# Performance work log

Hardware: AMD Instinct MI355X
Metric: run time of the kernel (lower is better)

Reference implementation:

```python
import jax, jax.numpy as jnp
import numpy as np

NBITS = 8
NUM_HEADS = 6


def _quant(x, alpha, nbits=NBITS):
    # LSQ-style fake quantization with straight-through estimator.
    qn = -(2 ** (nbits - 1))        # -128
    qp = 2 ** (nbits - 1) - 1       # 127
    s = jnp.clip(x / alpha, qn, qp)
    s = s + jax.lax.stop_gradient(jnp.round(s) - s)  # STE round
    return s * alpha


def setup_inputs() -> dict:
    key = jax.random.key(0)
    ks = jax.random.split(key, 12)
    B, N, C = 2, 2048, 384
    x = jax.random.normal(ks[0], (B, N, C), dtype=jnp.float32)
    w_qkv = jax.random.normal(ks[1], (3 * C, C), dtype=jnp.float32) * 0.02
    w_proj = jax.random.normal(ks[2], (C, C), dtype=jnp.float32) * 0.02
    b_proj = jnp.zeros((C,), dtype=jnp.float32)

    def alpha(k, lo, hi):
        return jax.random.uniform(k, (1,), dtype=jnp.float32, minval=lo, maxval=hi)

    return {
        "x": x,
        "w_qkv": w_qkv,
        "w_proj": w_proj,
        "b_proj": b_proj,
        "a_qkv_w": alpha(ks[3], 0.001, 0.005),
        "a_qkv_a": alpha(ks[4], 0.02, 0.05),
        "a_proj_w": alpha(ks[5], 0.001, 0.005),
        "a_proj_a": alpha(ks[6], 0.02, 0.05),
        "a_q": alpha(ks[7], 0.01, 0.03),
        "a_k": alpha(ks[8], 0.01, 0.03),
        "a_v": alpha(ks[9], 0.01, 0.03),
        "a_attn": alpha(ks[10], 0.01, 0.03),
        "a_attn2": alpha(ks[11], 0.005, 0.01),
    }


def reference(x, w_qkv, w_proj, b_proj, a_qkv_w, a_qkv_a, a_proj_w, a_proj_a,
              a_q, a_k, a_v, a_attn, a_attn2):
    B, N, C = x.shape
    H = NUM_HEADS
    D = C // H
    scale = D ** (-0.5)

    # quantized qkv linear (no bias)
    qkv = _quant(x, a_qkv_a) @ _quant(w_qkv, a_qkv_w).T          # [B,N,3C]
    qkv = qkv.reshape(B, N, 3, H, D).transpose(2, 0, 3, 1, 4)    # [3,B,H,N,D]
    q, k, v = qkv[0], qkv[1], qkv[2]
    q = _quant(q, a_q)
    k = _quant(k, a_k)
    v = _quant(v, a_v)

    attn = jnp.einsum("bhnd,bhmd->bhnm", q, k) * scale           # [B,H,N,N]
    attn = _quant(attn, a_attn)
    attn = jax.nn.softmax(attn, axis=-1)
    attn = _quant(attn, a_attn2)

    out = jnp.einsum("bhnm,bhmd->bhnd", attn, v)                 # [B,H,N,D]
    out = out.transpose(0, 2, 1, 3).reshape(B, N, C)

    # quantized output projection (with bias)
    out = _quant(out, a_proj_a) @ _quant(w_proj, a_proj_w).T + b_proj
    return out
```

## Files before the change

kernel.cpp:

```cpp
#include <hip/hip_runtime.h>
#include <math.h>


typedef int i32x4 __attribute__((ext_vector_type(4)));

#define MFMA_I8(a, b, c) __builtin_amdgcn_mfma_i32_16x16x64_i8(a, b, c, 0, 0, 0)

__device__ __forceinline__ float qclip(float s) {
  return fminf(fmaxf(s, -128.0f), 127.0f);
}

__device__ __forceinline__ float fdivn(float x, float c, float rc) {
  float q0 = x * rc;
  float e = fmaf(-c, q0, x);
  return fmaf(e, rc, q0);
}

__device__ __forceinline__ void quant16_body(const float* __restrict__ in,
                                             signed char* __restrict__ out,
                                             float a, int i) {
  const float4* p = (const float4*)in + 4 * (size_t)i;
  union { uint4 u; signed char c[16]; } o;
#pragma unroll
  for (int u = 0; u < 4; ++u) {
    float4 v = p[u];
    o.c[4 * u + 0] = (signed char)(int)rintf(qclip(v.x / a));
    o.c[4 * u + 1] = (signed char)(int)rintf(qclip(v.y / a));
    o.c[4 * u + 2] = (signed char)(int)rintf(qclip(v.z / a));
    o.c[4 * u + 3] = (signed char)(int)rintf(qclip(v.w / a));
  }
  *(uint4*)(out + 16 * (size_t)i) = o.u;
}

__global__ __launch_bounds__(256)
void prep(const float* __restrict__ x, const float* __restrict__ wqkv,
          const float* __restrict__ wproj,
          signed char* __restrict__ xq, signed char* __restrict__ wqq,
          signed char* __restrict__ wpq, float* __restrict__ E2,
          const float* __restrict__ a_qkv_a, const float* __restrict__ a_qkv_w,
          const float* __restrict__ a_proj_w, const float* __restrict__ aattn) {
  const int b = blockIdx.x, t = threadIdx.x;
  if (b < 384) {
    int i = b * 256 + t;
    if (i < 98304) quant16_body(x, xq, a_qkv_a[0], i);
  } else if (b < 492) {
    int i = (b - 384) * 256 + t;
    if (i < 27648) quant16_body(wqkv, wqq, a_qkv_w[0], i);
  } else if (b < 528) {
    int i = (b - 492) * 256 + t;
    if (i < 9216) quant16_body(wproj, wpq, a_proj_w[0], i);
  } else {
    int i = (b - 528) * 256 + t;
    float a = aattn[0];
    int vm = (i >> 8) - 128;
    int s = (i & 255) - 128;
    float m = a * (float)vm;
    E2[i] = expf(a * (float)s - m);
  }
}

__global__ __launch_bounds__(256)
void gemm_qkv(const signed char* __restrict__ A, const signed char* __restrict__ W,
              signed char* __restrict__ qws, signed char* __restrict__ kws,
              signed char* __restrict__ vwsT,
              const float* __restrict__ aa, const float* __restrict__ aw,
              const float* __restrict__ aq, const float* __restrict__ ak,
              const float* __restrict__ av) {
  const int t = threadIdx.x;
  const int w = t >> 6, lane = t & 63;
  const int lm = lane & 15, quad = lane >> 4;
  const int wm = w >> 1, wn = w & 1;
  const int m0 = blockIdx.x * 128 + wm * 64;
  const int n0 = blockIdx.y * 128 + wn * 64;
  i32x4 acc[4][4] = {};
  for (int k0 = 0; k0 < 384; k0 += 64) {
    i32x4 af[4], bf[4];
#pragma unroll
    for (int mt = 0; mt < 4; ++mt)
      af[mt] = *(const i32x4*)(A + (size_t)(m0 + mt * 16 + lm) * 384 + k0 + quad * 16);
#pragma unroll
    for (int nt = 0; nt < 4; ++nt)
      bf[nt] = *(const i32x4*)(W + (size_t)(n0 + nt * 16 + lm) * 384 + k0 + quad * 16);
#pragma unroll
    for (int mt = 0; mt < 4; ++mt)
#pragma unroll
      for (int nt = 0; nt < 4; ++nt)
        acc[mt][nt] = MFMA_I8(af[mt], bf[nt], acc[mt][nt]);
  }
  const float sAB = aa[0] * aw[0];
  const float vaq = aq[0], vak = ak[0], vav = av[0];
#pragma unroll
  for (int mt = 0; mt < 4; ++mt) {
#pragma unroll
    for (int nt = 0; nt < 4; ++nt) {
      int cg = n0 + nt * 16 + lm;
      int t3 = cg / 384;
      int rem = cg - t3 * 384;
      int h = rem >> 6, d = rem & 63;
#pragma unroll
      for (int r = 0; r < 4; ++r) {
        int m = m0 + mt * 16 + quad * 4 + r;
        int bb = m >> 11, nn = m & 2047;
        int bh = bb * 6 + h;
        float val = (float)acc[mt][nt][r] * sAB;
        if (t3 == 0) {
          qws[((size_t)(bh * 2048 + nn) << 6) + d] = (signed char)(int)rintf(qclip(val / vaq));
        } else if (t3 == 1) {
          kws[((size_t)(bh * 2048 + nn) << 6) + d] = (signed char)(int)rintf(qclip(val / vak));
        } else {
          vwsT[((size_t)((bh << 6) + d) << 11) + nn] = (signed char)(int)rintf(qclip(val / vav));
        }
      }
    }
  }
}

#define TROW 2064
__global__ __launch_bounds__(256)
void attn_fused(const signed char* __restrict__ qws, const signed char* __restrict__ kws,
                const signed char* __restrict__ vwsT, const float* __restrict__ E2,
                signed char* __restrict__ ows,
                const float* __restrict__ aq, const float* __restrict__ ak,
                const float* __restrict__ aattn, const float* __restrict__ aattn2,
                const float* __restrict__ av, const float* __restrict__ apa) {
  __shared__ signed char tileS[16 * TROW];
  __shared__ float EfS[16 * 257];
  const int t = threadIdx.x;
  const int w = t >> 6, lane = t & 63;
  const int lm = lane & 15, quad = lane >> 4;
  const int i0 = blockIdx.x * 16;
  const int bh = blockIdx.y;

  const signed char* Qb = qws + ((size_t)bh << 17);
  const signed char* Kb = kws + ((size_t)bh << 17);

  i32x4 bq = *(const i32x4*)(Qb + ((size_t)(i0 + lm) << 6) + quad * 16);
  const float sc = aq[0] * ak[0] * 0.125f;
  const float ia = aattn[0];
  const float ria = 1.0f / ia;
#pragma unroll 4
  for (int ct = 0; ct < 32; ++ct) {
    int col0 = (w << 9) + ct * 16;
    i32x4 akf = *(const i32x4*)(Kb + ((size_t)(col0 + lm) << 6) + quad * 16);
    i32x4 z = {};
    i32x4 acc = MFMA_I8(akf, bq, z);
    union { unsigned int u; signed char c[4]; } pk;
#pragma unroll
    for (int r = 0; r < 4; ++r) {
      float sv = (float)acc[r] * sc;
      pk.c[r] = (signed char)(int)rintf(qclip(fdivn(sv, ia, ria)));
    }
    *(unsigned int*)(tileS + lm * TROW + col0 + quad * 4) = pk.u;
  }
  __syncthreads();

  const float a2 = aattn2[0];
  int* lutI = (int*)EfS;
#pragma unroll
  for (int rr = 0; rr < 4; ++rr) {
    const int row = w * 4 + rr;
    const char4* prow = (const char4*)(tileS + row * TROW);
    char4 vals[8];
    int vmax = -129;
#pragma unroll
    for (int u = 0; u < 8; ++u) {
      vals[u] = prow[lane + (u << 6)];
      vmax = max(vmax, (int)vals[u].x);
      vmax = max(vmax, (int)vals[u].y);
      vmax = max(vmax, (int)vals[u].z);
      vmax = max(vmax, (int)vals[u].w);
    }
#pragma unroll
    for (int off = 32; off > 0; off >>= 1)
      vmax = max(vmax, __shfl_xor(vmax, off, 64));
    float efu[4];
#pragma unroll
    for (int u = 0; u < 4; ++u) {
      efu[u] = E2[((vmax + 128) << 8) + u * 64 + lane];
      EfS[row * 257 + u * 64 + lane] = efu[u];
    }
    const float* Er = EfS + row * 257 + 128;
    float l = 0.0f;
#pragma unroll
    for (int u = 0; u < 8; ++u) {
      l += Er[(int)vals[u].x];
      l += Er[(int)vals[u].y];
      l += Er[(int)vals[u].z];
      l += Er[(int)vals[u].w];
    }
#pragma unroll
    for (int off = 32; off > 0; off >>= 1)
      l += __shfl_xor(l, off, 64);
#pragma unroll
    for (int u = 0; u < 4; ++u) {
      int pq = (int)(signed char)(int)rintf(qclip(efu[u] / l / a2));
      lutI[row * 257 + u * 64 + lane] = pq;
    }
  }
  __syncthreads();

  i32x4 areg[8];
  {
    const int* lr = lutI + lm * 257 + 128;
    const signed char* srow = tileS + lm * TROW + (w << 9) + quad * 16;
#pragma unroll
    for (int js = 0; js < 8; ++js) {
      union { uint4 u; signed char c[16]; } sv;
      sv.u = *(const uint4*)(srow + js * 64);
      union { i32x4 v; signed char c[16]; } dv;
#pragma unroll
      for (int b = 0; b < 16; ++b) dv.c[b] = (signed char)lr[(int)sv.c[b]];
      areg[js] = dv.v;
    }
  }

  const signed char* Vb = vwsT + ((size_t)bh << 17) + (w << 9);
  i32x4 acc[4] = {};
#pragma unroll
  for (int js = 0; js < 8; ++js) {
    int j0 = js * 64;
    i32x4 bf[4];
#pragma unroll
    for (int nt = 0; nt < 4; ++nt)
      bf[nt] = *(const i32x4*)(Vb + ((size_t)(nt * 16 + lm) << 11) + j0 + quad * 16);
#pragma unroll
    for (int nt = 0; nt < 4; ++nt)
      acc[nt] = MFMA_I8(areg[js], bf[nt], acc[nt]);
  }

  int* red = (int*)tileS;
  __syncthreads();
  if (w > 0) {
    int* rw = red + (w - 1) * 1088 + lane * 17;
#pragma unroll
    for (int nt = 0; nt < 4; ++nt)
#pragma unroll
      for (int r = 0; r < 4; ++r)
        rw[nt * 4 + r] = acc[nt][r];
  }
  __syncthreads();
  if (w == 0) {
    const float so = a2 * av[0];
    const float ipa = apa[0];
    int bb = bh / 6, h = bh % 6;
#pragma unroll
    for (int nt = 0; nt < 4; ++nt) {
      int d = nt * 16 + lm;
#pragma unroll
      for (int r = 0; r < 4; ++r) {
        int s = acc[nt][r] + red[lane * 17 + nt * 4 + r]
              + red[1088 + lane * 17 + nt * 4 + r]
              + red[2176 + lane * 17 + nt * 4 + r];
        int i = i0 + quad * 4 + r;
        ows[(size_t)((bb << 11) + i) * 384 + (h << 6) + d] =
            (signed char)(int)rintf(qclip((float)s * so / ipa));
      }
    }
  }
}

__global__ __launch_bounds__(256)
void gemm_proj(const signed char* __restrict__ A, const signed char* __restrict__ W,
               const float* __restrict__ bias, float* __restrict__ out,
               const float* __restrict__ apa, const float* __restrict__ apw) {
  const int t = threadIdx.x;
  const int w = t >> 6, lane = t & 63;
  const int lm = lane & 15, quad = lane >> 4;
  const int wm = w >> 1, wn = w & 1;
  const int m0 = blockIdx.x * 64 + wm * 32;
  const int n0 = blockIdx.y * 64 + wn * 32;
  i32x4 acc[2][2] = {};
  for (int k0 = 0; k0 < 384; k0 += 64) {
    i32x4 af[2], bf[2];
#pragma unroll
    for (int mt = 0; mt < 2; ++mt)
      af[mt] = *(const i32x4*)(A + (size_t)(m0 + mt * 16 + lm) * 384 + k0 + quad * 16);
#pragma unroll
    for (int nt = 0; nt < 2; ++nt)
      bf[nt] = *(const i32x4*)(W + (size_t)(n0 + nt * 16 + lm) * 384 + k0 + quad * 16);
#pragma unroll
    for (int mt = 0; mt < 2; ++mt)
#pragma unroll
      for (int nt = 0; nt < 2; ++nt)
        acc[mt][nt] = MFMA_I8(af[mt], bf[nt], acc[mt][nt]);
  }
  const float sAB = apa[0] * apw[0];
#pragma unroll
  for (int mt = 0; mt < 2; ++mt) {
#pragma unroll
    for (int nt = 0; nt < 2; ++nt) {
      int cg = n0 + nt * 16 + lm;
#pragma unroll
      for (int r = 0; r < 4; ++r) {
        int m = m0 + mt * 16 + quad * 4 + r;
        out[(size_t)m * 384 + cg] = (float)acc[mt][nt][r] * sAB + bias[cg];
      }
    }
  }
}

extern "C" void kernel_launch(void* const* d_in, const int* in_sizes, int n_in,
                              void* d_out, int out_size, void* d_ws, size_t ws_size,
                              hipStream_t stream) {
  const float* x        = (const float*)d_in[0];
  const float* w_qkv    = (const float*)d_in[1];
  const float* w_proj   = (const float*)d_in[2];
  const float* b_proj   = (const float*)d_in[3];
  const float* a_qkv_w  = (const float*)d_in[4];
  const float* a_qkv_a  = (const float*)d_in[5];
  const float* a_proj_w = (const float*)d_in[6];
  const float* a_proj_a = (const float*)d_in[7];
  const float* a_q      = (const float*)d_in[8];
  const float* a_k      = (const float*)d_in[9];
  const float* a_v      = (const float*)d_in[10];
  const float* a_attn   = (const float*)d_in[11];
  const float* a_attn2  = (const float*)d_in[12];

  char* wsb = (char*)d_ws;
  signed char* xq   = (signed char*)(wsb + 0);
  signed char* wqq  = (signed char*)(wsb + 1572864);
  signed char* wpq  = (signed char*)(wsb + 2015232);
  signed char* qws  = (signed char*)(wsb + 2162688);
  signed char* kws  = (signed char*)(wsb + 3735552);
  signed char* vwsT = (signed char*)(wsb + 5308416);
  signed char* ows  = (signed char*)(wsb + 6881280);
  float*       E2   = (float*)(wsb + 8454144);

  prep<<<784, 256, 0, stream>>>(x, w_qkv, w_proj, xq, wqq, wpq, E2,
                                a_qkv_a, a_qkv_w, a_proj_w, a_attn);
  gemm_qkv<<<dim3(32, 9), 256, 0, stream>>>(xq, wqq, qws, kws, vwsT,
                                            a_qkv_a, a_qkv_w, a_q, a_k, a_v);
  attn_fused<<<dim3(128, 12), 256, 0, stream>>>(qws, kws, vwsT, E2, ows,
                                                a_q, a_k, a_attn, a_attn2,
                                                a_v, a_proj_a);
  gemm_proj<<<dim3(64, 6), 256, 0, stream>>>(ows, wpq, b_proj, (float*)d_out,
                                             a_proj_a, a_proj_w);
}
```

Before: 167.4 us.

## Split-K the QKV GEMM, replace divisions with reciprocal refinement, drop prob LUT

The QKV GEMM moves to 64x64 tiles with a two-way split-K across warps, reduced through shared memory, and launches four times as many blocks. This targets poor occupancy on a grid of only 288 blocks. All the quantization divisions become reciprocal multiplies with an FMA correction step. In attention, the quantized probabilities are computed directly per element and written back into the score tile, replacing the integer lookup-table pass. That adds per-element divide work while removing a 16-way byte gather per fragment.

```diff
diff --git a/kernel.cpp b/kernel.cpp
--- a/kernel.cpp
+++ b/kernel.cpp
@@ -19,15 +19,16 @@
 __device__ __forceinline__ void quant16_body(const float* __restrict__ in,
                                              signed char* __restrict__ out,
                                              float a, int i) {
+  const float ra = 1.0f / a;
   const float4* p = (const float4*)in + 4 * (size_t)i;
   union { uint4 u; signed char c[16]; } o;
 #pragma unroll
   for (int u = 0; u < 4; ++u) {
     float4 v = p[u];
-    o.c[4 * u + 0] = (signed char)(int)rintf(qclip(v.x / a));
-    o.c[4 * u + 1] = (signed char)(int)rintf(qclip(v.y / a));
-    o.c[4 * u + 2] = (signed char)(int)rintf(qclip(v.z / a));
-    o.c[4 * u + 3] = (signed char)(int)rintf(qclip(v.w / a));
+    o.c[4 * u + 0] = (signed char)(int)rintf(qclip(fdivn(v.x, a, ra)));
+    o.c[4 * u + 1] = (signed char)(int)rintf(qclip(fdivn(v.y, a, ra)));
+    o.c[4 * u + 2] = (signed char)(int)rintf(qclip(fdivn(v.z, a, ra)));
+    o.c[4 * u + 3] = (signed char)(int)rintf(qclip(fdivn(v.w, a, ra)));
   }
   *(uint4*)(out + 16 * (size_t)i) = o.u;
 }
@@ -66,49 +67,71 @@
               const float* __restrict__ aa, const float* __restrict__ aw,
               const float* __restrict__ aq, const float* __restrict__ ak,
               const float* __restrict__ av) {
+  __shared__ int red[2 * 64 * 33];
   const int t = threadIdx.x;
   const int w = t >> 6, lane = t & 63;
   const int lm = lane & 15, quad = lane >> 4;
-  const int wm = w >> 1, wn = w & 1;
-  const int m0 = blockIdx.x * 128 + wm * 64;
-  const int n0 = blockIdx.y * 128 + wn * 64;
-  i32x4 acc[4][4] = {};
-  for (int k0 = 0; k0 < 384; k0 += 64) {
-    i32x4 af[4], bf[4];
+  const int kw = w >> 1, nw = w & 1;
+  const int m0 = blockIdx.x * 64;
+  const int n0 = blockIdx.y * 64 + nw * 32;
+  i32x4 acc[4][2] = {};
+#pragma unroll
+  for (int kk = 0; kk < 3; ++kk) {
+    int k0 = kw * 192 + kk * 64;
+    i32x4 af[4], bf[2];
 #pragma unroll
     for (int mt = 0; mt < 4; ++mt)
       af[mt] = *(const i32x4*)(A + (size_t)(m0 + mt * 16 + lm) * 384 + k0 + quad * 16);
 #pragma unroll
-    for (int nt = 0; nt < 4; ++nt)
+    for (int nt = 0; nt < 2; ++nt)
       bf[nt] = *(const i32x4*)(W + (size_t)(n0 + nt * 16 + lm) * 384 + k0 + quad * 16);
 #pragma unroll
     for (int mt = 0; mt < 4; ++mt)
 #pragma unroll
-      for (int nt = 0; nt < 4; ++nt)
+      for (int nt = 0; nt < 2; ++nt)
         acc[mt][nt] = MFMA_I8(af[mt], bf[nt], acc[mt][nt]);
   }
-  const float sAB = aa[0] * aw[0];
-  const float vaq = aq[0], vak = ak[0], vav = av[0];
-#pragma unroll
-  for (int mt = 0; mt < 4; ++mt) {
-#pragma unroll
-    for (int nt = 0; nt < 4; ++nt) {
-      int cg = n0 + nt * 16 + lm;
-      int t3 = cg / 384;
-      int rem = cg - t3 * 384;
-      int h = rem >> 6, d = rem & 63;
-#pragma unroll
-      for (int r = 0; r < 4; ++r) {
-        int m = m0 + mt * 16 + quad * 4 + r;
-        int bb = m >> 11, nn = m & 2047;
-        int bh = bb * 6 + h;
-        float val = (float)acc[mt][nt][r] * sAB;
-        if (t3 == 0) {
-          qws[((size_t)(bh * 2048 + nn) << 6) + d] = (signed char)(int)rintf(qclip(val / vaq));
-        } else if (t3 == 1) {
-          kws[((size_t)(bh * 2048 + nn) << 6) + d] = (signed char)(int)rintf(qclip(val / vak));
-        } else {
-          vwsT[((size_t)((bh << 6) + d) << 11) + nn] = (signed char)(int)rintf(qclip(val / vav));
+  if (kw == 1) {
+    int* rw = red + nw * 2112 + lane * 33;
+#pragma unroll
+    for (int mt = 0; mt < 4; ++mt)
+#pragma unroll
+      for (int nt = 0; nt < 2; ++nt)
+#pragma unroll
+        for (int r = 0; r < 4; ++r)
+          rw[mt * 8 + nt * 4 + r] = acc[mt][nt][r];
+  }
+  __syncthreads();
+  if (kw == 0) {
+    const int* rw = red + nw * 2112 + lane * 33;
+    const float sAB = aa[0] * aw[0];
+    const float vaq = aq[0], vak = ak[0], vav = av[0];
+    const float rq = 1.0f / vaq, rk = 1.0f / vak, rv = 1.0f / vav;
+#pragma unroll
+    for (int mt = 0; mt < 4; ++mt) {
+#pragma unroll
+      for (int nt = 0; nt < 2; ++nt) {
+        int cg = n0 + nt * 16 + lm;
+        int t3 = cg / 384;
+        int rem = cg - t3 * 384;
+        int h = rem >> 6, d = rem & 63;
+#pragma unroll
+        for (int r = 0; r < 4; ++r) {
+          int m = m0 + mt * 16 + quad * 4 + r;
+          int bb = m >> 11, nn = m & 2047;
+          int bh = bb * 6 + h;
+          int sum = acc[mt][nt][r] + rw[mt * 8 + nt * 4 + r];
+          float val = (float)sum * sAB;
+          if (t3 == 0) {
+            qws[((size_t)(bh * 2048 + nn) << 6) + d] =
+                (signed char)(int)rintf(qclip(fdivn(val, vaq, rq)));
+          } else if (t3 == 1) {
+            kws[((size_t)(bh * 2048 + nn) << 6) + d] =
+                (signed char)(int)rintf(qclip(fdivn(val, vak, rk)));
+          } else {
+            vwsT[((size_t)((bh << 6) + d) << 11) + nn] =
+                (signed char)(int)rintf(qclip(fdivn(val, vav, rv)));
+          }
         }
       }
     }
@@ -155,11 +178,11 @@
   __syncthreads();
 
   const float a2 = aattn2[0];
-  int* lutI = (int*)EfS;
+  const float ra2 = 1.0f / a2;
 #pragma unroll
   for (int rr = 0; rr < 4; ++rr) {
     const int row = w * 4 + rr;
-    const char4* prow = (const char4*)(tileS + row * TROW);
+    char4* prow = (char4*)(tileS + row * TROW);
     char4 vals[8];
     int vmax = -129;
 #pragma unroll
@@ -173,47 +196,47 @@
 #pragma unroll
     for (int off = 32; off > 0; off >>= 1)
       vmax = max(vmax, __shfl_xor(vmax, off, 64));
-    float efu[4];
-#pragma unroll
-    for (int u = 0; u < 4; ++u) {
-      efu[u] = E2[((vmax + 128) << 8) + u * 64 + lane];
-      EfS[row * 257 + u * 64 + lane] = efu[u];
-    }
+#pragma unroll
+    for (int u = 0; u < 4; ++u)
+      EfS[row * 257 + u * 64 + lane] = E2[((vmax + 128) << 8) + u * 64 + lane];
     const float* Er = EfS + row * 257 + 128;
+    float ge[8][4];
     float l = 0.0f;
 #pragma unroll
     for (int u = 0; u < 8; ++u) {
-      l += Er[(int)vals[u].x];
-      l += Er[(int)vals[u].y];
-      l += Er[(int)vals[u].z];
-      l += Er[(int)vals[u].w];
+      ge[u][0] = Er[(int)vals[u].x];
+      ge[u][1] = Er[(int)vals[u].y];
+      ge[u][2] = Er[(int)vals[u].z];
+      ge[u][3] = Er[(int)vals[u].w];
+      l += ge[u][0];
+      l += ge[u][1];
+      l += ge[u][2];
+      l += ge[u][3];
     }
 #pragma unroll
     for (int off = 32; off > 0; off >>= 1)
       l += __shfl_xor(l, off, 64);
-#pragma unroll
-    for (int u = 0; u < 4; ++u) {
-      int pq = (int)(signed char)(int)rintf(qclip(efu[u] / l / a2));
-      lutI[row * 257 + u * 64 + lane] = pq;
+    const float rl = 1.0f / l;
+#pragma unroll
+    for (int u = 0; u < 8; ++u) {
+      union { unsigned int ui; signed char c[4]; } pk;
+#pragma unroll
+      for (int c = 0; c < 4; ++c) {
+        float tq = fdivn(ge[u][c], l, rl);
+        pk.c[c] = (signed char)(int)rintf(qclip(fdivn(tq, a2, ra2)));
+      }
+      *(unsigned int*)(prow + lane + (u << 6)) = pk.ui;
     }
   }
   __syncthreads();
 
   i32x4 areg[8];
   {
-    const int* lr = lutI + lm * 257 + 128;
     const signed char* srow = tileS + lm * TROW + (w << 9) + quad * 16;
 #pragma unroll
-    for (int js = 0; js < 8; ++js) {
-      union { uint4 u; signed char c[16]; } sv;
-      sv.u = *(const uint4*)(srow + js * 64);
-      union { i32x4 v; signed char c[16]; } dv;
-#pragma unroll
-      for (int b = 0; b < 16; ++b) dv.c[b] = (signed char)lr[(int)sv.c[b]];
-      areg[js] = dv.v;
-    }
-  }
-
+    for (int js = 0; js < 8; ++js)
+      areg[js] = *(const i32x4*)(srow + js * 64);
+  }
   const signed char* Vb = vwsT + ((size_t)bh << 17) + (w << 9);
   i32x4 acc[4] = {};
 #pragma unroll
@@ -242,6 +265,7 @@
   if (w == 0) {
     const float so = a2 * av[0];
     const float ipa = apa[0];
+    const float ripa = 1.0f / ipa;
     int bb = bh / 6, h = bh % 6;
 #pragma unroll
     for (int nt = 0; nt < 4; ++nt) {
@@ -253,7 +277,7 @@
               + red[2176 + lane * 17 + nt * 4 + r];
         int i = i0 + quad * 4 + r;
         ows[(size_t)((bb << 11) + i) * 384 + (h << 6) + d] =
-            (signed char)(int)rintf(qclip((float)s * so / ipa));
+            (signed char)(int)rintf(qclip(fdivn((float)s * so, ipa, ripa)));
       }
     }
   }
@@ -328,8 +352,8 @@
 
   prep<<<784, 256, 0, stream>>>(x, w_qkv, w_proj, xq, wqq, wpq, E2,
                                 a_qkv_a, a_qkv_w, a_proj_w, a_attn);
-  gemm_qkv<<<dim3(32, 9), 256, 0, stream>>>(xq, wqq, qws, kws, vwsT,
-                                            a_qkv_a, a_qkv_w, a_q, a_k, a_v);
+  gemm_qkv<<<dim3(64, 18), 256, 0, stream>>>(xq, wqq, qws, kws, vwsT,
+                                             a_qkv_a, a_qkv_w, a_q, a_k, a_v);
   attn_fused<<<dim3(128, 12), 256, 0, stream>>>(qws, kws, vwsT, E2, ows,
                                                 a_q, a_k, a_attn, a_attn2,
                                                 a_v, a_proj_a);
```

Measured after the change: 158.1 us. -5.6%, faster.
